# Performance work log

Measured on AMD Instinct MI355X. Metric: run time of the kernel, lower is better.

## Reference

```python
import jax, jax.numpy as jnp
import numpy as np

N = 50000
E = 400000
C_IN = 32
H = 64
RATIO = 0.5
SEQ_LEN = 5


def setup_inputs() -> dict:
    key = jax.random.key(0)
    ks = jax.random.split(key, 12)
    x = jax.random.normal(ks[0], (N, C_IN), jnp.float32)
    row = jax.random.randint(ks[1], (E,), 0, N, jnp.int32)
    off = jax.random.randint(ks[2], (E,), 1, N, jnp.int32)
    col = ((row + off) % N).astype(jnp.int32)  # no self-loops
    edge_index = jnp.stack([row, col])
    mask = jax.random.uniform(ks[3], (N,)) < 0.5

    def g(k, shape, fan):
        return jax.random.normal(k, shape, jnp.float32) / np.float32(np.sqrt(fan))

    return {
        "x": x, "edge_index": edge_index, "mask": mask,
        "conv0_w": g(ks[4], (C_IN, H), C_IN), "conv0_b": jnp.zeros((H,), jnp.float32),
        "conv1_w": g(ks[5], (H, H), H), "conv1_b": jnp.zeros((H,), jnp.float32),
        "pool_w": g(ks[6], (H,), H),
        "up_w": g(ks[7], (H, H), H), "up_b": jnp.zeros((H,), jnp.float32),
        "lstm0_w_ih": g(ks[8], (4 * H, H), H), "lstm0_w_hh": g(ks[9], (4 * H, H), H),
        "lstm0_b_ih": jnp.zeros((4 * H,), jnp.float32), "lstm0_b_hh": jnp.zeros((4 * H,), jnp.float32),
        "fin_w_ih": g(ks[10], (4 * H, H), H), "fin_w_hh": g(ks[11], (4 * H, H), H),
        "fin_b_ih": jnp.zeros((4 * H,), jnp.float32), "fin_b_hh": jnp.zeros((4 * H,), jnp.float32),
    }


def _coalesce(row, col, w, n):
    # sum duplicate (row, col) entries; output sorted by (row, col)
    key = row.astype(np.int64) * n + col.astype(np.int64)
    uk, inv = np.unique(key, return_inverse=True)
    w2 = np.bincount(inv, weights=w.astype(np.float64), minlength=uk.shape[0]).astype(np.float32)
    return uk // n, uk % n, w2


def _augment_adj(row, col, w, n):
    # remove self loops, add self loops (weight 1), compute A @ A (sparse), remove self loops
    m = row != col
    row = np.concatenate([row[m].astype(np.int64), np.arange(n, dtype=np.int64)])
    col = np.concatenate([col[m].astype(np.int64), np.arange(n, dtype=np.int64)])
    w = np.concatenate([w[m].astype(np.float32), np.ones(n, np.float32)])
    row, col, w = _coalesce(row, col, w, n)  # CSR-ordered
    cnt = np.bincount(row, minlength=n)
    indptr = np.concatenate([[0], np.cumsum(cnt)])
    dk = cnt[col]                      # out-degree of middle node k for each edge (i,k)
    starts = indptr[col]
    total = int(dk.sum())
    seg = np.repeat(np.cumsum(dk) - dk, dk)
    gi = np.repeat(starts, dk) + (np.arange(total) - seg)
    oi = np.repeat(row, dk)
    oj = col[gi]
    ow = np.repeat(w, dk) * w[gi]
    r2, c2, w2 = _coalesce(oi, oj, ow, n)
    m2 = r2 != c2
    return r2[m2], c2[m2], w2[m2]


def _gcn(x, row, col, ew, n, W, b):
    # GCNConv(improved=True): self-loop weight 2.0, symmetric deg^-1/2 normalization,
    # aggregate messages at target (col)
    h = x @ W
    loop = jnp.arange(n, dtype=row.dtype)
    r = jnp.concatenate([row, loop])
    c = jnp.concatenate([col, loop])
    w = jnp.concatenate([ew, jnp.full((n,), 2.0, ew.dtype)])
    deg = jax.ops.segment_sum(w, c, num_segments=n)
    dinv = jnp.where(deg > 0, jax.lax.rsqrt(deg), 0.0)
    norm = dinv[r] * w * dinv[c]
    out = jax.ops.segment_sum(norm[:, None] * h[r], c, num_segments=n)
    return out + b


def _sequences(x, mi):
    # sliding window [idx-L+1, idx] per masked node, zero left-padded
    t = mi[:, None] + jnp.arange(SEQ_LEN)[None, :] - (SEQ_LEN - 1)  # [M, L]
    return jnp.where((t >= 0)[:, :, None], x[jnp.clip(t, 0)], 0.0)


def _lstm_last(seq, w_ih, w_hh, b_ih, b_hh):
    # torch LSTM gate order: i, f, g, o; zero init state; return last hidden
    h = jnp.zeros((seq.shape[0], w_hh.shape[1]), seq.dtype)
    c = jnp.zeros_like(h)
    def step(carry, xt):
        h, c = carry
        g = xt @ w_ih.T + h @ w_hh.T + b_ih + b_hh
        i, f, gg, o = jnp.split(g, 4, axis=-1)
        c = jax.nn.sigmoid(f) * c + jax.nn.sigmoid(i) * jnp.tanh(gg)
        h = jax.nn.sigmoid(o) * jnp.tanh(c)
        return (h, c), None
    (h, _), _ = jax.lax.scan(step, (h, c), jnp.swapaxes(seq, 0, 1))
    return h


def reference(x, edge_index, mask, conv0_w, conv0_b, conv1_w, conv1_b, pool_w,
              up_w, up_b, lstm0_w_ih, lstm0_w_hh, lstm0_b_ih, lstm0_b_hh,
              fin_w_ih, fin_w_hh, fin_b_ih, fin_b_hh):
    n = x.shape[0]
    row0, col0 = edge_index[0], edge_index[1]
    ew0 = jnp.ones((row0.shape[0],), x.dtype)

    # down conv 0
    x1 = jax.nn.relu(_gcn(x, row0, col0, ew0, n, conv0_w, conv0_b))

    # augment_adj: sparse (A+I)^2 without diagonal (structural, constant)
    r2, c2, w2 = _augment_adj(np.asarray(row0), np.asarray(col0),
                              np.ones(row0.shape[0], np.float32), n)

    # TopKPooling: score = tanh((x.w)/||w||), keep top ceil(ratio*n)
    score = jnp.tanh((x1 @ pool_w) / jnp.linalg.norm(pool_w))
    k = int(np.ceil(RATIO * n))
    perm = np.argsort(-np.asarray(score), kind="stable")[:k]
    remap = np.full(n, -1, np.int64)
    remap[perm] = np.arange(k)
    keep = (remap[r2] >= 0) & (remap[c2] >= 0)
    pr = jnp.asarray(remap[r2[keep]].astype(np.int32))
    pc = jnp.asarray(remap[c2[keep]].astype(np.int32))
    pw = jnp.asarray(w2[keep])
    permj = jnp.asarray(perm.astype(np.int32))
    xp = x1[permj] * score[permj][:, None]

    # down conv 1 on pooled graph
    x2 = jax.nn.relu(_gcn(xp, pr, pc, pw, k, conv1_w, conv1_b))

    # up path (depth=1): LSTM over skip features at masked nodes
    mi = jnp.asarray(np.where(np.asarray(mask))[0].astype(np.int32))
    h0 = _lstm_last(_sequences(x1, mi), lstm0_w_ih, lstm0_w_hh, lstm0_b_ih, lstm0_b_hh)
    res = x1.at[mi].set(h0)
    up = jnp.zeros_like(x1).at[permj].set(x2)
    xo = _gcn(res + up, row0, col0, ew0, n, up_w, up_b)  # last level: no activation

    # final LSTM on masked nodes
    hf = _lstm_last(_sequences(xo, mi), fin_w_ih, fin_w_hh, fin_b_ih, fin_b_hh)
    return xo.at[mi].set(hf)
```

## Files before the change

### kernel.cpp

```cpp
#include <hip/hip_runtime.h>
#include <math.h>

#define NN 50000
#define EE 400000
#define CINV 32
#define KKEEP 25000
#define SEQL 5
#define HASH_BITS 20
#define HASH_SIZE (1u<<HASH_BITS)
#define HASH_MASK (HASH_SIZE-1u)
#define HEMPTY 0xFFFFFFFFu
#define PSB 196

typedef float vf4 __attribute__((ext_vector_type(4)));

__device__ __forceinline__ float sigm(float x){ return __builtin_amdgcn_rcpf(1.f+__expf(-x)); }
__device__ __forceinline__ float ftanh(float x){ return 1.f - 2.f*__builtin_amdgcn_rcpf(1.f+__expf(2.f*x)); }

__global__ void k_init(uint2* __restrict__ hash, unsigned* __restrict__ hist,
                       int* __restrict__ degcnt, int* __restrict__ diagint,
                       int* __restrict__ fillc,
                       unsigned* scal, unsigned long long* selp,
                       const float* __restrict__ w0, const float* __restrict__ b0i,
                       const float* __restrict__ b0h, const float* __restrict__ wf,
                       const float* __restrict__ bfi, const float* __restrict__ bfh,
                       float* __restrict__ WT0, float* __restrict__ WTf,
                       float* __restrict__ bs0, float* __restrict__ bsf){
  int i = blockIdx.x*256 + threadIdx.x;
  if (i < (int)HASH_SIZE) hash[i] = make_uint2(HEMPTY, 0u);
  if (i < 4*65536) hist[i] = 0u;
  if (i < NN){ degcnt[i]=0; diagint[i]=0; fillc[i]=0; }
  if (i < 256*64){
    int r = i>>6, k = i&63;
    int dst = k*256 + (r&63)*4 + (r>>6);
    WT0[dst] = w0[i];
    WTf[dst] = wf[i];
  }
  if (i < 256){
    int dst = (i&63)*4 + (i>>6);
    bs0[dst]=b0i[i]+b0h[i]; bsf[dst]=bfi[i]+bfh[i];
  }
  if (i == 0){ scal[0]=0u; scal[1]=0u; scal[3]=KKEEP; selp[0]=0ull; }
}

__global__ void k_phase2(const int* __restrict__ row, const int* __restrict__ col,
                         const int* __restrict__ mp, int* __restrict__ degcnt,
                         uint2* __restrict__ tab, unsigned* scal,
                         const float* __restrict__ X, const float* __restrict__ W,
                         float* __restrict__ Y){
  int idx = blockIdx.x*256 + threadIdx.x;
  if (idx < EE){
    int c = col[idx];
    atomicAdd(&degcnt[c], 1);
    unsigned key = (unsigned)row[idx]*50000u + (unsigned)c;
    unsigned h = (key*2654435761u) >> (32-HASH_BITS);
    for(;;){
      unsigned old = atomicCAS(&tab[h].x, HEMPTY, key);
      if (old==HEMPTY || old==key){ atomicAdd(&tab[h].y, 1u); break; }
      h = (h+1)&HASH_MASK;
    }
  }
  if (idx < NN/4){ if ((unsigned)mp[idx] > 1u) atomicOr(&scal[1], 1u); }
  if (idx < NN*16){
    int i = idx>>4, fq = idx&15;
    const vf4* X4 = (const vf4*)&X[i*CINV];
    const vf4* W4 = (const vf4*)W;
    vf4 acc = {0.f,0.f,0.f,0.f};
    #pragma unroll
    for (int kq=0;kq<CINV/4;kq++){
      vf4 xv = X4[kq];
      #pragma unroll
      for (int u=0;u<4;u++) acc += xv[u] * W4[(kq*4+u)*16+fq];
    }
    ((vf4*)Y)[i*16+fq] = acc;
  }
}

__global__ void k_psum1(const int* __restrict__ deg, const void* __restrict__ mp,
                        const unsigned* __restrict__ scal,
                        int* __restrict__ part, int* __restrict__ bsum,
                        int* __restrict__ mpart, int* __restrict__ mbsum,
                        float* __restrict__ dinv){
  __shared__ int sc[256];
  __shared__ int sm[256];
  int b = blockIdx.x, t = threadIdx.x, i = b*256+t;
  int v = (i<NN) ? deg[i] : 0;
  int mv = 0;
  if (i < NN){
    dinv[i] = rsqrtf((float)v + 2.0f);
    mv = scal[1] ? (int)(((const unsigned char*)mp)[i] != 0)
                 : (int)(((const int*)mp)[i] != 0);
  }
  sc[t] = v; sm[t] = mv; __syncthreads();
  for (int o=1;o<256;o<<=1){
    int x = (t>=o) ? sc[t-o] : 0;
    int y = (t>=o) ? sm[t-o] : 0;
    __syncthreads();
    sc[t] += x; sm[t] += y;
    __syncthreads();
  }
  if (i < NN){ part[i] = sc[t]-v; mpart[i] = sm[t]-mv; }
  if (t == 255){ bsum[b] = sc[255]; mbsum[b] = sm[255]; }
}
__global__ void k_psum3(const int* __restrict__ part, const int* __restrict__ bsum,
                        const int* __restrict__ mpart, const int* __restrict__ mbsum,
                        const void* __restrict__ mp, unsigned* __restrict__ scal,
                        int* __restrict__ indptr, int* __restrict__ mlist,
                        int* __restrict__ minv){
  __shared__ int sc[256];
  __shared__ int sm[256];
  int t = threadIdx.x;
  int v = (t<PSB) ? bsum[t] : 0;
  int w = (t<PSB) ? mbsum[t] : 0;
  sc[t] = v; sm[t] = w; __syncthreads();
  for (int o=1;o<256;o<<=1){
    int x = (t>=o) ? sc[t-o] : 0;
    int y = (t>=o) ? sm[t-o] : 0;
    __syncthreads();
    sc[t] += x; sm[t] += y;
    __syncthreads();
  }
  int bb = blockIdx.x;
  int ex  = sc[bb] - ((bb<PSB) ? bsum[bb] : 0);
  int mex = sm[bb] - ((bb<PSB) ? mbsum[bb] : 0);
  int i = bb*256 + t;
  if (i < NN){
    indptr[i] = part[i] + ex;
    int mv = scal[1] ? (int)(((const unsigned char*)mp)[i] != 0)
                     : (int)(((const int*)mp)[i] != 0);
    if (mv){ int p = mpart[i] + mex; mlist[p] = i; minv[i] = p; }
    else minv[i] = -1;
  }
  if (i == 0){ indptr[NN] = EE; scal[0] = (unsigned)sm[255]; }
}

__global__ void k_phase4(const int* __restrict__ row, const int* __restrict__ col,
                         const int* __restrict__ indptr, int* __restrict__ fillc,
                         int* __restrict__ csr_r, const uint2* __restrict__ tab,
                         int* __restrict__ diagint){
  int idx = blockIdx.x*256 + threadIdx.x;
  if (idx >= EE) return;
  int r = row[idx], c = col[idx];
  int pos = indptr[c] + atomicAdd(&fillc[c], 1);
  csr_r[pos] = r;
  unsigned rkey = (unsigned)c*50000u + (unsigned)r;
  unsigned h = (rkey*2654435761u) >> (32-HASH_BITS);
  for(;;){
    unsigned kk = tab[h].x;
    if (kk==rkey){ atomicAdd(&diagint[r], (int)tab[h].y); break; }
    if (kk==HEMPTY) break;
    h = (h+1)&HASH_MASK;
  }
}

__global__ void g_gcn0(const int* __restrict__ indptr, const int* __restrict__ csr_r,
                       const float* __restrict__ dinv, const float* __restrict__ H,
                       const float* __restrict__ b, const float* __restrict__ pw,
                       float* __restrict__ out, unsigned long long* __restrict__ keys,
                       float* __restrict__ score, unsigned* __restrict__ hist){
  int node = blockIdx.x*4 + (threadIdx.x>>6), lane = threadIdx.x&63;
  if (node >= NN) return;
  int s = __builtin_amdgcn_readfirstlane(indptr[node]);
  int e = __builtin_amdgcn_readfirstlane(indptr[node+1]);
  int deg = e - s;
  float a0=0.f,a1=0.f,a2=0.f,a3=0.f,a4=0.f,a5=0.f,a6=0.f,a7=0.f;
  for (int base=0; base<deg; base+=64){
    int take = min(64, deg-base);
    bool act = lane < take;
    int ii = act ? csr_r[s+base+lane] : 0;
    float dv = act ? dinv[ii] : 0.f;
    for (int j=0; j<take; j+=8){
      int   r0=__shfl(ii,j,64),   r1=__shfl(ii,j+1,64), r2=__shfl(ii,j+2,64), r3=__shfl(ii,j+3,64),
            r4=__shfl(ii,j+4,64), r5=__shfl(ii,j+5,64), r6=__shfl(ii,j+6,64), r7=__shfl(ii,j+7,64);
      float d0=__shfl(dv,j,64),   d1=__shfl(dv,j+1,64), d2=__shfl(dv,j+2,64), d3=__shfl(dv,j+3,64),
            d4=__shfl(dv,j+4,64), d5=__shfl(dv,j+5,64), d6=__shfl(dv,j+6,64), d7=__shfl(dv,j+7,64);
      a0 += d0*H[(size_t)r0*64+lane];
      a1 += d1*H[(size_t)r1*64+lane];
      a2 += d2*H[(size_t)r2*64+lane];
      a3 += d3*H[(size_t)r3*64+lane];
      a4 += d4*H[(size_t)r4*64+lane];
      a5 += d5*H[(size_t)r5*64+lane];
      a6 += d6*H[(size_t)r6*64+lane];
      a7 += d7*H[(size_t)r7*64+lane];
    }
  }
  float acc = ((a0+a1)+(a2+a3)) + ((a4+a5)+(a6+a7));
  float di = dinv[node];
  float v = di*acc + 2.f*di*di*H[(size_t)node*64+lane] + b[lane];
  float x1v = fmaxf(v, 0.f);
  out[(size_t)node*64+lane] = x1v;
  float pv = pw[lane];
  float nq = pv*pv;
  float dq = x1v*pv;
  for (int o=32;o;o>>=1){ nq += __shfl_down(nq, o, 64); dq += __shfl_down(dq, o, 64); }
  if (lane==0){
    float sv = tanhf(dq / sqrtf(nq));
    sv = sv + 0.0f;
    score[node] = sv;
    unsigned u = __float_as_uint(sv);
    unsigned asc = (u>>31) ? ~u : (u | 0x80000000u);
    unsigned desc = ~asc;
    keys[node] = (((unsigned long long)desc)<<32) | (unsigned)node;
    atomicAdd(&hist[desc>>16], 1u);
  }
}
__global__ void g_t2(const int* __restrict__ indptr, const int* __restrict__ csr_r,
                     const float* __restrict__ dinv1, const float* __restrict__ hp,
                     float* __restrict__ t2){
  int node = blockIdx.x*4 + (threadIdx.x>>6), lane = threadIdx.x&63;
  if (node >= NN) return;
  int s = __builtin_amdgcn_readfirstlane(indptr[node]);
  int e = __builtin_amdgcn_readfirstlane(indptr[node+1]);
  int deg = e - s;
  float a0 = dinv1[node]*hp[(size_t)node*64+lane];
  float a1=0.f,a2=0.f,a3=0.f,a4=0.f,a5=0.f,a6=0.f,a7=0.f;
  for (int base=0; base<deg; base+=64){
    int take = min(64, deg-base);
    bool act = lane < take;
    int ii = act ? csr_r[s+base+lane] : 0;
    float dv = act ? dinv1[ii] : 0.f;
    for (int j=0; j<take; j+=8){
      int   r0=__shfl(ii,j,64),   r1=__shfl(ii,j+1,64), r2=__shfl(ii,j+2,64), r3=__shfl(ii,j+3,64),
            r4=__shfl(ii,j+4,64), r5=__shfl(ii,j+5,64), r6=__shfl(ii,j+6,64), r7=__shfl(ii,j+7,64);
      float d0=__shfl(dv,j,64),   d1=__shfl(dv,j+1,64), d2=__shfl(dv,j+2,64), d3=__shfl(dv,j+3,64),
            d4=__shfl(dv,j+4,64), d5=__shfl(dv,j+5,64), d6=__shfl(dv,j+6,64), d7=__shfl(dv,j+7,64);
      a0 += d0*hp[(size_t)r0*64+lane];
      a1 += d1*hp[(size_t)r1*64+lane];
      a2 += d2*hp[(size_t)r2*64+lane];
      a3 += d3*hp[(size_t)r3*64+lane];
      a4 += d4*hp[(size_t)r4*64+lane];
      a5 += d5*hp[(size_t)r5*64+lane];
      a6 += d6*hp[(size_t)r6*64+lane];
      a7 += d7*hp[(size_t)r7*64+lane];
    }
  }
  t2[(size_t)node*64+lane] = ((a0+a1)+(a2+a3)) + ((a4+a5)+(a6+a7));
}
__global__ void g_agg2m(const int* __restrict__ indptr, const int* __restrict__ csr_r,
                        const float* __restrict__ t2, float* __restrict__ hp,
                        const float* __restrict__ dinv1, const int* __restrict__ diagint,
                        const int* __restrict__ kp, const float* __restrict__ b1,
                        const float* __restrict__ C, const float* __restrict__ Hbuf,
                        const int* __restrict__ minv, const float* __restrict__ Wu){
  __shared__ __align__(16) float shD[4][64];
  int wv = threadIdx.x>>6, lane = threadIdx.x&63;
  int node = blockIdx.x*4 + wv;
  if (node >= NN) return;
  int mv = minv[node];
  float base = (mv >= 0) ? Hbuf[(size_t)mv*64+lane] : C[(size_t)node*64+lane];
  float add = 0.f;
  if (kp[node]){
    int s = __builtin_amdgcn_readfirstlane(indptr[node]);
    int e = __builtin_amdgcn_readfirstlane(indptr[node+1]);
    int deg = e - s;
    float a0 = t2[(size_t)node*64+lane];
    float a1=0.f,a2=0.f,a3=0.f,a4=0.f,a5=0.f,a6=0.f,a7=0.f;
    for (int bs2=0; bs2<deg; bs2+=64){
      int take = min(64, deg-bs2);
      bool act = lane < take;
      int ii = act ? csr_r[s+bs2+lane] : 0;
      float wvp = act ? 1.f : 0.f;
      for (int j=0; j<take; j+=8){
        int   r0=__shfl(ii,j,64),   r1=__shfl(ii,j+1,64), r2=__shfl(ii,j+2,64), r3=__shfl(ii,j+3,64),
              r4=__shfl(ii,j+4,64), r5=__shfl(ii,j+5,64), r6=__shfl(ii,j+6,64), r7=__shfl(ii,j+7,64);
        float w0=__shfl(wvp,j,64),  w1=__shfl(wvp,j+1,64), w2=__shfl(wvp,j+2,64), w3=__shfl(wvp,j+3,64),
              w4=__shfl(wvp,j+4,64), w5=__shfl(wvp,j+5,64), w6=__shfl(wvp,j+6,64), w7=__shfl(wvp,j+7,64);
        a0 += w0*t2[(size_t)r0*64+lane];
        a1 += w1*t2[(size_t)r1*64+lane];
        a2 += w2*t2[(size_t)r2*64+lane];
        a3 += w3*t2[(size_t)r3*64+lane];
        a4 += w4*t2[(size_t)r4*64+lane];
        a5 += w5*t2[(size_t)r5*64+lane];
        a6 += w6*t2[(size_t)r6*64+lane];
        a7 += w7*t2[(size_t)r7*64+lane];
      }
    }
    float acc = ((a0+a1)+(a2+a3)) + ((a4+a5)+(a6+a7));
    float di = dinv1[node], hv = hp[(size_t)node*64+lane];
    float diag = (float)(diagint[node] + 1);
    float v = di*(acc - diag*di*hv) + 2.f*di*di*hv + b1[lane];
    add = fmaxf(v, 0.f);
  }
  float dval = base + add;
  shD[wv][lane] = dval;
  asm volatile("s_waitcnt lgkmcnt(0)" ::: "memory");
  __builtin_amdgcn_sched_barrier(0);
  float acc = 0.f;
  #pragma unroll 16
  for (int k=0;k<64;k++) acc += shD[wv][k] * Wu[k*64 + lane];
  hp[(size_t)node*64+lane] = acc;
}
__global__ void g_up(const int* __restrict__ indptr, const int* __restrict__ csr_r,
                     const float* __restrict__ dinv, const float* __restrict__ H,
                     const float* __restrict__ b, float* __restrict__ xo, float* __restrict__ out){
  int node = blockIdx.x*4 + (threadIdx.x>>6), lane = threadIdx.x&63;
  if (node >= NN) return;
  int s = __builtin_amdgcn_readfirstlane(indptr[node]);
  int e = __builtin_amdgcn_readfirstlane(indptr[node+1]);
  int deg = e - s;
  float a0=0.f,a1=0.f,a2=0.f,a3=0.f,a4=0.f,a5=0.f,a6=0.f,a7=0.f;
  for (int base=0; base<deg; base+=64){
    int take = min(64, deg-base);
    bool act = lane < take;
    int ii = act ? csr_r[s+base+lane] : 0;
    float dv = act ? dinv[ii] : 0.f;
    for (int j=0; j<take; j+=8){
      int   r0=__shfl(ii,j,64),   r1=__shfl(ii,j+1,64), r2=__shfl(ii,j+2,64), r3=__shfl(ii,j+3,64),
            r4=__shfl(ii,j+4,64), r5=__shfl(ii,j+5,64), r6=__shfl(ii,j+6,64), r7=__shfl(ii,j+7,64);
      float d0=__shfl(dv,j,64),   d1=__shfl(dv,j+1,64), d2=__shfl(dv,j+2,64), d3=__shfl(dv,j+3,64),
            d4=__shfl(dv,j+4,64), d5=__shfl(dv,j+5,64), d6=__shfl(dv,j+6,64), d7=__shfl(dv,j+7,64);
      a0 += d0*H[(size_t)r0*64+lane];
      a1 += d1*H[(size_t)r1*64+lane];
      a2 += d2*H[(size_t)r2*64+lane];
      a3 += d3*H[(size_t)r3*64+lane];
      a4 += d4*H[(size_t)r4*64+lane];
      a5 += d5*H[(size_t)r5*64+lane];
      a6 += d6*H[(size_t)r6*64+lane];
      a7 += d7*H[(size_t)r7*64+lane];
    }
  }
  float acc = ((a0+a1)+(a2+a3)) + ((a4+a5)+(a6+a7));
  float di = dinv[node];
  float v = di*acc + 2.f*di*di*H[(size_t)node*64+lane] + b[lane];
  xo[(size_t)node*64+lane] = v; out[(size_t)node*64+lane] = v;
}

__global__ void k_hist(const unsigned long long* __restrict__ keys, unsigned* __restrict__ hist,
                       const unsigned long long* __restrict__ selp, int round){
  int i = blockIdx.x*256 + threadIdx.x;
  if (i >= NN) return;
  unsigned long long key = keys[i];
  int shift = 48 - 16*round;
  if ((key>>(shift+16)) == selp[0])
    atomicAdd(&hist[(unsigned)((key>>shift)&0xFFFFull)], 1u);
}
__global__ void k_pick(const unsigned* __restrict__ hist, unsigned long long* selp, unsigned* scal){
  __shared__ unsigned csum[256];
  __shared__ unsigned bins[256];
  __shared__ int schunk;
  int t = threadIdx.x;
  const uint4* h4 = (const uint4*)(hist + t*256);
  unsigned s = 0;
  #pragma unroll 8
  for (int j=0;j<64;j++){ uint4 v = h4[j]; s += v.x+v.y+v.z+v.w; }
  csum[t] = s;
  __syncthreads();
  if (t==0){
    unsigned rem = scal[3];
    int chunk = 255;
    for (int c2=0;c2<256;c2++){ unsigned cc=csum[c2]; if (rem>cc) rem-=cc; else { chunk=c2; break; } }
    schunk = chunk; scal[3] = rem;
  }
  __syncthreads();
  bins[t] = hist[schunk*256 + t];
  __syncthreads();
  if (t==0){
    unsigned rem = scal[3];
    int bin = schunk*256 + 255;
    for (int b=0;b<256;b++){ unsigned hv=bins[b]; if (rem>hv) rem-=hv; else { bin = schunk*256 + b; break; } }
    selp[0] = (selp[0]<<16) | (unsigned long long)(unsigned)bin;
    scal[3] = rem;
  }
}
__global__ void k_tsg(const int* __restrict__ indptr, const int* __restrict__ csr_r,
                      const unsigned long long* __restrict__ keys,
                      const unsigned long long* __restrict__ selp,
                      int* __restrict__ kp, int* __restrict__ ts){
  int i = blockIdx.x*256 + threadIdx.x;
  if (i >= NN) return;
  unsigned long long sp = selp[0];
  int s = indptr[i], e = indptr[i+1];
  int self = (keys[i] <= sp) ? 1 : 0;
  kp[i] = self;
  int acc = self;
  for (int j=s;j<e;j++) acc += (keys[csr_r[j]] <= sp) ? 1 : 0;
  ts[i] = acc;
}
__global__ void k_csgmm(const int* __restrict__ indptr, const int* __restrict__ csr_r,
                        const int* __restrict__ ts, const int* __restrict__ diagint,
                        const int* __restrict__ kp, float* __restrict__ dinv1,
                        const float* __restrict__ X, const float* __restrict__ W,
                        const float* __restrict__ sc, float* __restrict__ Y){
  int idx = blockIdx.x*256 + threadIdx.x;
  if (idx < NN*16){
    int i = idx>>4, fq = idx&15;
    if (!kp[i]){ vf4 z = {0.f,0.f,0.f,0.f}; ((vf4*)Y)[i*16+fq] = z; return; }
    const vf4* X4 = (const vf4*)&X[i*64];
    const vf4* W4 = (const vf4*)W;
    vf4 acc = {0.f,0.f,0.f,0.f};
    #pragma unroll
    for (int kq=0;kq<16;kq++){
      vf4 xv = X4[kq];
      #pragma unroll
      for (int u=0;u<4;u++) acc += xv[u] * W4[(kq*4+u)*16+fq];
    }
    acc *= sc[i];
    ((vf4*)Y)[i*16+fq] = acc;
  } else {
    int i = idx - NN*16;
    if (i >= NN) return;
    int s = indptr[i], e = indptr[i+1];
    int acc = ts[i];
    for (int j=s;j<e;j++) acc += ts[csr_r[j]];
    dinv1[i] = kp[i] ? rsqrtf((float)(acc - diagint[i] - 1) + 2.0f) : 0.f;
  }
}

__global__ __launch_bounds__(256) void k_xw(const float* __restrict__ src,
        const float* __restrict__ WT, const float* __restrict__ bsum,
        float* __restrict__ XW){
  __shared__ vf4 Wl[4096];
  int t = threadIdx.x;
  const vf4* Wg = (const vf4*)WT;
  for (int u=t; u<4096; u+=256) Wl[u] = Wg[u];
  int fq = t & 63, wv = t >> 6;
  vf4 bias = ((const vf4*)bsum)[fq];
  __syncthreads();
  for (int g = blockIdx.x*4 + wv; g < NN/4; g += gridDim.x*4){
    int n0 = g*4;
    const vf4* X4 = (const vf4*)&src[(size_t)n0*64];
    vf4 a0=bias, a1=bias, a2=bias, a3=bias;
    #pragma unroll 4
    for (int kq=0;kq<16;kq++){
      vf4 x0 = X4[kq], x1 = X4[16+kq], x2 = X4[32+kq], x3 = X4[48+kq];
      vf4 w0 = Wl[(kq*4+0)*64+fq];
      vf4 w1 = Wl[(kq*4+1)*64+fq];
      vf4 w2 = Wl[(kq*4+2)*64+fq];
      vf4 w3 = Wl[(kq*4+3)*64+fq];
      a0 += x0.x*w0 + x0.y*w1 + x0.z*w2 + x0.w*w3;
      a1 += x1.x*w0 + x1.y*w1 + x1.z*w2 + x1.w*w3;
      a2 += x2.x*w0 + x2.y*w1 + x2.z*w2 + x2.w*w3;
      a3 += x3.x*w0 + x3.y*w1 + x3.z*w2 + x3.w*w3;
    }
    vf4* Y = (vf4*)XW;
    Y[(size_t)n0*64 + fq]       = a0;
    Y[(size_t)n0*64 + 64 + fq]  = a1;
    Y[(size_t)n0*64 + 128 + fq] = a2;
    Y[(size_t)n0*64 + 192 + fq] = a3;
  }
}

__global__ __launch_bounds__(256) void k_rec(const float* __restrict__ XW,
        const float* __restrict__ whh, const float* __restrict__ bsum,
        const int* __restrict__ mlist, const unsigned* __restrict__ scal,
        float* __restrict__ dst, int scatter){
  int M = (int)scal[0];
  if (M < 0 || M > NN) M = 0;
  int task = blockIdx.x;
  if (task*4 >= M) return;
  int w = threadIdx.x>>6, lane = threadIdx.x&63;
  int r = w*64 + lane;
  const vf4* g4 = (const vf4*)&whh[(size_t)r*64];
  vf4 wh[16];
  #pragma unroll
  for (int j=0;j<16;j++) wh[j] = g4[j];
  __shared__ float sh[4][64];
  __shared__ float gates[4][4][64];
  int m = task*4 + w;
  bool valid = (m < M);
  int node = mlist[valid ? m : (M-1)];
  node = min(max(node, 0), NN-1);
  const vf4* XW4 = (const vf4*)XW;
  vf4 bp = ((const vf4*)bsum)[lane];
  vf4 xs0, xs1, xs2, xs3, xs4;
  {
    int r0 = node - 4, r1 = node - 3;
    xs0 = (r0 >= 0) ? XW4[(size_t)r0*64 + lane] : bp;
    xs1 = (r1 >= 0) ? XW4[(size_t)r1*64 + lane] : bp;
  }
  float c, h;
  c = sigm(xs0.x)*ftanh(xs0.z);
  h = sigm(xs0.w)*ftanh(c);
  sh[w][lane] = h;
  __syncthreads();
  #pragma unroll
  for (int t=1;t<SEQL;t++){
    if (t==1){ int ri = node-2; xs2 = (ri>=0) ? XW4[(size_t)ri*64+lane] : bp; }
    if (t==2){ int ri = node-1; xs3 = (ri>=0) ? XW4[(size_t)ri*64+lane] : bp; }
    if (t==3){ xs4 = XW4[(size_t)node*64 + lane]; }
    vf4 a0={0,0,0,0}, a1={0,0,0,0}, a2={0,0,0,0}, a3={0,0,0,0};
    #pragma unroll
    for (int j=0;j<16;j++){
      vf4 wj = wh[j];
      a0 += (*(const vf4*)&sh[0][j*4]) * wj;
      a1 += (*(const vf4*)&sh[1][j*4]) * wj;
      a2 += (*(const vf4*)&sh[2][j*4]) * wj;
      a3 += (*(const vf4*)&sh[3][j*4]) * wj;
    }
    gates[0][w][lane] = a0.x+a0.y+a0.z+a0.w;
    gates[1][w][lane] = a1.x+a1.y+a1.z+a1.w;
    gates[2][w][lane] = a2.x+a2.y+a2.z+a2.w;
    gates[3][w][lane] = a3.x+a3.y+a3.z+a3.w;
    __syncthreads();
    vf4 xv = (t==1) ? xs1 : (t==2) ? xs2 : (t==3) ? xs3 : xs4;
    float gi = gates[w][0][lane] + xv.x;
    float gf = gates[w][1][lane] + xv.y;
    float gg = gates[w][2][lane] + xv.z;
    float go = gates[w][3][lane] + xv.w;
    c = sigm(gf)*c + sigm(gi)*ftanh(gg);
    h = sigm(go)*ftanh(c);
    sh[w][lane] = h;
    __syncthreads();
  }
  if (valid){
    size_t o = scatter ? ((size_t)node*64 + lane) : ((size_t)m*64 + lane);
    dst[o] = h;
  }
}

extern "C" void kernel_launch(void* const* d_in, const int* in_sizes, int n_in,
                              void* d_out, int out_size, void* d_ws, size_t ws_size,
                              hipStream_t stream) {
  const float* x   = (const float*)d_in[0];
  const int*   ei  = (const int*)d_in[1];
  const int*   row = ei;
  const int*   col = ei + EE;
  const void*  mp  = d_in[2];
  const float* W0  = (const float*)d_in[3];
  const float* b0  = (const float*)d_in[4];
  const float* W1  = (const float*)d_in[5];
  const float* b1  = (const float*)d_in[6];
  const float* pw  = (const float*)d_in[7];
  const float* Wu  = (const float*)d_in[8];
  const float* bu  = (const float*)d_in[9];
  const float* l0wih=(const float*)d_in[10];
  const float* l0whh=(const float*)d_in[11];
  const float* l0bih=(const float*)d_in[12];
  const float* l0bhh=(const float*)d_in[13];
  const float* lfwih=(const float*)d_in[14];
  const float* lfwhh=(const float*)d_in[15];
  const float* lfbih=(const float*)d_in[16];
  const float* lfbhh=(const float*)d_in[17];

  char* wp = (char*)d_ws;
  auto alloc = [&](size_t bytes)->char*{ char* p = wp; wp += ((bytes+255)/256)*256; return p; };
  float* A     = (float*)alloc((size_t)NN*64*4);
  float* B     = (float*)alloc((size_t)NN*64*4);
  float* C     = (float*)alloc((size_t)NN*64*4);
  float* Ebuf  = (float*)alloc((size_t)NN*64*4);
  float* Hbuf  = (float*)alloc((size_t)NN*64*4);
  float* XW    = (float*)alloc((size_t)NN*256*4);
  float* WT0   = (float*)alloc((size_t)256*64*4);
  float* WTf   = (float*)alloc((size_t)256*64*4);
  float* bs0   = (float*)alloc((size_t)256*4);
  float* bsf   = (float*)alloc((size_t)256*4);
  float* score = (float*)alloc((size_t)NN*4);
  float* dinv0 = (float*)alloc((size_t)NN*4);
  float* dinv1 = (float*)alloc((size_t)NN*4);
  unsigned long long* keys = (unsigned long long*)alloc((size_t)NN*8);
  int* degcnt  = (int*)alloc((size_t)NN*4);
  int* diagint = (int*)alloc((size_t)NN*4);
  int* ts      = (int*)alloc((size_t)NN*4);
  int* kp      = (int*)alloc((size_t)NN*4);
  int* mlist   = (int*)alloc((size_t)NN*4);
  int* minv    = (int*)alloc((size_t)NN*4);
  int* indptr  = (int*)alloc((size_t)(NN+1)*4);
  int* part    = (int*)alloc((size_t)NN*4);
  int* mpart   = (int*)alloc((size_t)NN*4);
  int* fillc   = (int*)alloc((size_t)NN*4);
  int* bsum    = (int*)alloc((size_t)256*4);
  int* mbsum   = (int*)alloc((size_t)256*4);
  int* csr_r   = (int*)alloc((size_t)EE*4);
  uint2* hash  = (uint2*)alloc((size_t)HASH_SIZE*8);
  unsigned* hist=(unsigned*)alloc((size_t)4*65536*4);
  unsigned* scal=(unsigned*)alloc(256);
  unsigned long long* selp = (unsigned long long*)(scal + 4);

  #define GRID1(n) dim3(((n)+255)/256), dim3(256), 0, stream
  #define GRIDW dim3((NN+3)/4), dim3(256), 0, stream

  k_init<<<GRID1(HASH_SIZE)>>>(hash, hist, degcnt, diagint, fillc,
                               scal, selp, l0wih, l0bih, l0bhh, lfwih, lfbih, lfbhh,
                               WT0, WTf, bs0, bsf);
  k_phase2<<<GRID1(NN*16)>>>(row, col, (const int*)mp, degcnt, hash, scal, x, W0, A);
  k_psum1<<<dim3(PSB),dim3(256),0,stream>>>(degcnt, mp, scal, part, bsum, mpart, mbsum, dinv0);
  k_psum3<<<dim3(PSB),dim3(256),0,stream>>>(part, bsum, mpart, mbsum, mp, scal, indptr, mlist, minv);
  k_phase4<<<GRID1(EE)>>>(row, col, indptr, fillc, csr_r, hash, diagint);

  g_gcn0<<<GRIDW>>>(indptr, csr_r, dinv0, A, b0, pw, C, keys, score, hist);

  k_pick<<<dim3(1),dim3(256),0,stream>>>(hist, selp, scal);
  for (int r2=1;r2<4;r2++){
    k_hist<<<GRID1(NN)>>>(keys, hist + r2*65536, selp, r2);
    k_pick<<<dim3(1),dim3(256),0,stream>>>(hist + r2*65536, selp, scal);
  }
  k_tsg<<<GRID1(NN)>>>(indptr, csr_r, keys, selp, kp, ts);
  k_csgmm<<<GRID1(NN*16+NN)>>>(indptr, csr_r, ts, diagint, kp, dinv1, C, W1, score, Ebuf);
  g_t2<<<GRIDW>>>(indptr, csr_r, dinv1, Ebuf, A);

  k_xw<<<dim3(512),dim3(256),0,stream>>>(C, WT0, bs0, XW);
  k_rec<<<dim3(12500),dim3(256),0,stream>>>(XW, l0whh, bs0, mlist, scal, Hbuf, 0);

  g_agg2m<<<GRIDW>>>(indptr, csr_r, A, Ebuf, dinv1, diagint, kp, b1, C, Hbuf, minv, Wu);

  g_up<<<GRIDW>>>(indptr, csr_r, dinv0, Ebuf, bu, B, (float*)d_out);

  k_xw<<<dim3(512),dim3(256),0,stream>>>(B, WTf, bsf, XW);
  k_rec<<<dim3(12500),dim3(256),0,stream>>>(XW, lfwhh, bsf, mlist, scal, (float*)d_out, 1);
  #undef GRIDW
  #undef GRID1
}
```

Baseline: 619.6 us.

## Fuse radix top-k selection rounds into one kernel with grid barriers, overlap LSTM input GEMM

```diff
diff --git a/kernel.cpp b/kernel.cpp
--- a/kernel.cpp
+++ b/kernel.cpp
@@ -40,7 +40,11 @@
     int dst = (i&63)*4 + (i>>6);
     bs0[dst]=b0i[i]+b0h[i]; bsf[dst]=bfi[i]+bfh[i];
   }
-  if (i == 0){ scal[0]=0u; scal[1]=0u; scal[3]=KKEEP; selp[0]=0ull; }
+  if (i == 0){
+    scal[0]=0u; scal[1]=0u; scal[3]=KKEEP; selp[0]=0ull;
+    #pragma unroll
+    for (int q=8;q<16;q++) scal[q]=0u;
+  }
 }
 
 __global__ void k_phase2(const int* __restrict__ row, const int* __restrict__ col,
@@ -204,6 +208,140 @@
     atomicAdd(&hist[desc>>16], 1u);
   }
 }
+
+__global__ __launch_bounds__(256) void k_selxw(
+        unsigned* __restrict__ hist, const unsigned long long* __restrict__ keys,
+        unsigned long long* __restrict__ selp, unsigned* __restrict__ scal,
+        const int* __restrict__ indptr, const int* __restrict__ csr_r,
+        int* __restrict__ kp, int* __restrict__ ts,
+        const float* __restrict__ src, const float* __restrict__ WT,
+        const float* __restrict__ bsum, float* __restrict__ XW){
+  __shared__ vf4 Wl[4096];
+  int t = threadIdx.x, bid = blockIdx.x;
+  if (bid >= PSB){
+    const vf4* Wg = (const vf4*)WT;
+    for (int u=t; u<4096; u+=256) Wl[u] = Wg[u];
+    int fq = t & 63, wv = t >> 6;
+    vf4 bias = ((const vf4*)bsum)[fq];
+    __syncthreads();
+    for (int g = (bid-PSB)*4 + wv; g < NN/4; g += 512*4){
+      int n0 = g*4;
+      const vf4* X4 = (const vf4*)&src[(size_t)n0*64];
+      vf4 a0=bias, a1=bias, a2=bias, a3=bias;
+      #pragma unroll 4
+      for (int kq=0;kq<16;kq++){
+        vf4 x0 = X4[kq], x1 = X4[16+kq], x2 = X4[32+kq], x3 = X4[48+kq];
+        vf4 w0 = Wl[(kq*4+0)*64+fq];
+        vf4 w1 = Wl[(kq*4+1)*64+fq];
+        vf4 w2 = Wl[(kq*4+2)*64+fq];
+        vf4 w3 = Wl[(kq*4+3)*64+fq];
+        a0 += x0.x*w0 + x0.y*w1 + x0.z*w2 + x0.w*w3;
+        a1 += x1.x*w0 + x1.y*w1 + x1.z*w2 + x1.w*w3;
+        a2 += x2.x*w0 + x2.y*w1 + x2.z*w2 + x2.w*w3;
+        a3 += x3.x*w0 + x3.y*w1 + x3.z*w2 + x3.w*w3;
+      }
+      vf4* Y = (vf4*)XW;
+      Y[(size_t)n0*64 + fq]       = a0;
+      Y[(size_t)n0*64 + 64 + fq]  = a1;
+      Y[(size_t)n0*64 + 128 + fq] = a2;
+      Y[(size_t)n0*64 + 192 + fq] = a3;
+    }
+    return;
+  }
+  unsigned* csum = (unsigned*)&Wl[0];
+  unsigned* bins = (unsigned*)&Wl[64];
+  __shared__ unsigned long long spfx_sh;
+  __shared__ unsigned rem_sh;
+  __shared__ int schunk;
+  unsigned* syncc = scal + 8;
+  #define GBAR(idx) do { \
+    __syncthreads(); \
+    if (t==0){ \
+      __threadfence(); \
+      atomicAdd(&syncc[idx], 1u); \
+      while (atomicAdd(&syncc[idx], 0u) < (unsigned)PSB) __builtin_amdgcn_s_sleep(2); \
+    } \
+    __syncthreads(); \
+  } while(0)
+  if (bid == 0){
+    unsigned s = 0;
+    for (int j=0;j<256;j++) s += atomicAdd(&hist[t*256+j], 0u);
+    csum[t] = s;
+    __syncthreads();
+    if (t==0){
+      unsigned rem = KKEEP;
+      int chunk = 255;
+      for (int c2=0;c2<256;c2++){ unsigned cc=csum[c2]; if (rem>cc) rem-=cc; else { chunk=c2; break; } }
+      schunk = chunk; rem_sh = rem;
+    }
+    __syncthreads();
+    bins[t] = atomicAdd(&hist[schunk*256 + t], 0u);
+    __syncthreads();
+    if (t==0){
+      unsigned rem = rem_sh;
+      int bin = schunk*256 + 255;
+      for (int b2=0;b2<256;b2++){ unsigned hv=bins[b2]; if (rem>hv) rem-=hv; else { bin = schunk*256 + b2; break; } }
+      spfx_sh = (unsigned long long)(unsigned)bin;
+      rem_sh = rem;
+      atomicExch(selp, spfx_sh);
+    }
+    __syncthreads();
+  }
+  GBAR(0);
+  for (int r=1; r<4; r++){
+    unsigned long long sp = atomicAdd(selp, 0ull);
+    unsigned* hr = hist + r*65536;
+    int shift = 48 - 16*r;
+    {
+      int i = bid*256 + t;
+      if (i < NN){
+        unsigned long long key = keys[i];
+        if ((key>>(shift+16)) == sp)
+          atomicAdd(&hr[(unsigned)((key>>shift)&0xFFFFull)], 1u);
+      }
+    }
+    GBAR(2*r-1);
+    if (bid == 0){
+      unsigned s = 0;
+      for (int j=0;j<256;j++) s += atomicAdd(&hr[t*256+j], 0u);
+      csum[t] = s;
+      __syncthreads();
+      if (t==0){
+        unsigned rem = rem_sh;
+        int chunk = 255;
+        for (int c2=0;c2<256;c2++){ unsigned cc=csum[c2]; if (rem>cc) rem-=cc; else { chunk=c2; break; } }
+        schunk = chunk; rem_sh = rem;
+      }
+      __syncthreads();
+      bins[t] = atomicAdd(&hr[schunk*256 + t], 0u);
+      __syncthreads();
+      if (t==0){
+        unsigned rem = rem_sh;
+        int bin = schunk*256 + 255;
+        for (int b2=0;b2<256;b2++){ unsigned hv=bins[b2]; if (rem>hv) rem-=hv; else { bin = schunk*256 + b2; break; } }
+        spfx_sh = (spfx_sh<<16) | (unsigned long long)(unsigned)bin;
+        rem_sh = rem;
+        atomicExch(selp, spfx_sh);
+      }
+      __syncthreads();
+    }
+    GBAR(2*r);
+  }
+  #undef GBAR
+  {
+    unsigned long long sp = atomicAdd(selp, 0ull);
+    int i = bid*256 + t;
+    if (i < NN){
+      int s = indptr[i], e = indptr[i+1];
+      int self = (keys[i] <= sp) ? 1 : 0;
+      kp[i] = self;
+      int acc = self;
+      for (int j=s;j<e;j++) acc += (keys[csr_r[j]] <= sp) ? 1 : 0;
+      ts[i] = acc;
+    }
+  }
+}
+
 __global__ void g_t2(const int* __restrict__ indptr, const int* __restrict__ csr_r,
                      const float* __restrict__ dinv1, const float* __restrict__ hp,
                      float* __restrict__ t2){
@@ -325,57 +463,6 @@
   xo[(size_t)node*64+lane] = v; out[(size_t)node*64+lane] = v;
 }
 
-__global__ void k_hist(const unsigned long long* __restrict__ keys, unsigned* __restrict__ hist,
-                       const unsigned long long* __restrict__ selp, int round){
-  int i = blockIdx.x*256 + threadIdx.x;
-  if (i >= NN) return;
-  unsigned long long key = keys[i];
-  int shift = 48 - 16*round;
-  if ((key>>(shift+16)) == selp[0])
-    atomicAdd(&hist[(unsigned)((key>>shift)&0xFFFFull)], 1u);
-}
-__global__ void k_pick(const unsigned* __restrict__ hist, unsigned long long* selp, unsigned* scal){
-  __shared__ unsigned csum[256];
-  __shared__ unsigned bins[256];
-  __shared__ int schunk;
-  int t = threadIdx.x;
-  const uint4* h4 = (const uint4*)(hist + t*256);
-  unsigned s = 0;
-  #pragma unroll 8
-  for (int j=0;j<64;j++){ uint4 v = h4[j]; s += v.x+v.y+v.z+v.w; }
-  csum[t] = s;
-  __syncthreads();
-  if (t==0){
-    unsigned rem = scal[3];
-    int chunk = 255;
-    for (int c2=0;c2<256;c2++){ unsigned cc=csum[c2]; if (rem>cc) rem-=cc; else { chunk=c2; break; } }
-    schunk = chunk; scal[3] = rem;
-  }
-  __syncthreads();
-  bins[t] = hist[schunk*256 + t];
-  __syncthreads();
-  if (t==0){
-    unsigned rem = scal[3];
-    int bin = schunk*256 + 255;
-    for (int b=0;b<256;b++){ unsigned hv=bins[b]; if (rem>hv) rem-=hv; else { bin = schunk*256 + b; break; } }
-    selp[0] = (selp[0]<<16) | (unsigned long long)(unsigned)bin;
-    scal[3] = rem;
-  }
-}
-__global__ void k_tsg(const int* __restrict__ indptr, const int* __restrict__ csr_r,
-                      const unsigned long long* __restrict__ keys,
-                      const unsigned long long* __restrict__ selp,
-                      int* __restrict__ kp, int* __restrict__ ts){
-  int i = blockIdx.x*256 + threadIdx.x;
-  if (i >= NN) return;
-  unsigned long long sp = selp[0];
-  int s = indptr[i], e = indptr[i+1];
-  int self = (keys[i] <= sp) ? 1 : 0;
-  kp[i] = self;
-  int acc = self;
-  for (int j=s;j<e;j++) acc += (keys[csr_r[j]] <= sp) ? 1 : 0;
-  ts[i] = acc;
-}
 __global__ void k_csgmm(const int* __restrict__ indptr, const int* __restrict__ csr_r,
                         const int* __restrict__ ts, const int* __restrict__ diagint,
                         const int* __restrict__ kp, float* __restrict__ dinv1,
@@ -579,16 +666,13 @@
 
   g_gcn0<<<GRIDW>>>(indptr, csr_r, dinv0, A, b0, pw, C, keys, score, hist);
 
-  k_pick<<<dim3(1),dim3(256),0,stream>>>(hist, selp, scal);
-  for (int r2=1;r2<4;r2++){
-    k_hist<<<GRID1(NN)>>>(keys, hist + r2*65536, selp, r2);
-    k_pick<<<dim3(1),dim3(256),0,stream>>>(hist + r2*65536, selp, scal);
-  }
-  k_tsg<<<GRID1(NN)>>>(indptr, csr_r, keys, selp, kp, ts);
+  k_selxw<<<dim3(PSB+512),dim3(256),0,stream>>>(hist, keys, selp, scal,
+                                                indptr, csr_r, kp, ts,
+                                                C, WT0, bs0, XW);
+
   k_csgmm<<<GRID1(NN*16+NN)>>>(indptr, csr_r, ts, diagint, kp, dinv1, C, W1, score, Ebuf);
   g_t2<<<GRIDW>>>(indptr, csr_r, dinv1, Ebuf, A);
 
-  k_xw<<<dim3(512),dim3(256),0,stream>>>(C, WT0, bs0, XW);
   k_rec<<<dim3(12500),dim3(256),0,stream>>>(XW, l0whh, bs0, mlist, scal, Hbuf, 0);
 
   g_agg2m<<<GRIDW>>>(indptr, csr_r, A, Ebuf, dinv1, diagint, kp, b1, C, Hbuf, minv, Wu);
```

Result: slower. 715.4 us (+15.5%).
